# Kernel tuning notes

Hardware: AMD Instinct MI355X
Metric: run time of the kernel (lower is better)

The kernel has to match this reference:

```python
import jax, jax.numpy as jnp
import numpy as np

K = 3
STRIDE = 1
PAD = 1
DIL = 1


def setup_inputs() -> dict:
    key = jax.random.key(0)
    k1, k2, k3 = jax.random.split(key, 3)
    B, C, O, H, W = 8, 64, 64, 128, 128
    x = jax.random.normal(k1, (B, C, H, W), dtype=jnp.float32)
    # small offset-conv weights so predicted offsets stay in a sane range
    w_off = jax.random.normal(k2, (2 * K * K, C, K, K), dtype=jnp.float32) * 0.05
    b_off = jnp.zeros((2 * K * K,), dtype=jnp.float32)
    w_conv = jax.random.normal(k3, (O, C, K, K), dtype=jnp.float32) * (1.0 / np.sqrt(C * K * K))
    return {"x": x, "w_off": w_off, "b_off": b_off, "w_conv": w_conv}


def _offset_conv(x, w, b):
    y = jax.lax.conv_general_dilated(
        x, w, window_strides=(STRIDE, STRIDE),
        padding=[(PAD, PAD), (PAD, PAD)], rhs_dilation=(DIL, DIL),
        dimension_numbers=("NCHW", "OIHW", "NCHW"))
    return y + b[None, :, None, None]


def _deform_conv2d(x, offset, weight):
    # torchvision deform_conv2d v1, groups=1, offset_groups=1, no bias
    B, C, H, W = x.shape
    Ho, Wo = offset.shape[2], offset.shape[3]
    # offset channels laid out as (ky, kx, [dy, dx]) pairs
    off = offset.reshape(B, K, K, 2, Ho, Wo)
    dy, dx = off[:, :, :, 0], off[:, :, :, 1]           # [B,K,K,Ho,Wo]

    hs = (jnp.arange(Ho) * STRIDE - PAD).astype(offset.dtype)
    ws = (jnp.arange(Wo) * STRIDE - PAD).astype(offset.dtype)
    kk = (jnp.arange(K) * DIL).astype(offset.dtype)
    py = hs[None, None, None, :, None] + kk[None, :, None, None, None] + dy
    px = ws[None, None, None, None, :] + kk[None, None, :, None, None] + dx

    y0 = jnp.floor(py)
    x0 = jnp.floor(px)
    ly = py - y0
    lx = px - x0
    y0i = y0.astype(jnp.int32)
    x0i = x0.astype(jnp.int32)

    xf = x.reshape(B, C, H * W)

    def gather(yi, xi):
        valid = ((yi >= 0) & (yi < H) & (xi >= 0) & (xi < W)).astype(x.dtype)
        idx = jnp.clip(yi, 0, H - 1) * W + jnp.clip(xi, 0, W - 1)  # [B,K,K,Ho,Wo]
        idxf = idx.reshape(B, 1, -1)
        v = jnp.take_along_axis(xf, idxf, axis=2)                  # [B,C,K*K*Ho*Wo]
        v = v.reshape(B, C, K, K, Ho, Wo)
        return v * valid[:, None]                                  # zero-pad out of bounds

    ly_ = ly[:, None]  # broadcast over channel dim
    lx_ = lx[:, None]
    val = (gather(y0i, x0i) * (1 - ly_) * (1 - lx_)
           + gather(y0i, x0i + 1) * (1 - ly_) * lx_
           + gather(y0i + 1, x0i) * ly_ * (1 - lx_)
           + gather(y0i + 1, x0i + 1) * ly_ * lx_)   # [B,C,K,K,Ho,Wo]

    return jnp.einsum("bcklhw,ockl->bohw", val, weight)


def reference(x, w_off, b_off, w_conv):
    offset = _offset_conv(x, w_off, b_off)
    return _deform_conv2d(x, offset, w_conv)
```

## Files before the change

kernel.cpp:

```cpp
#include <hip/hip_runtime.h>

#define B_    8
#define C_    64
#define O_    64
#define H_    128
#define W_    128
#define HW_   (H_ * W_)
#define NOFF_ 18
#define KK_   9
#define TW_   19
#define PADW_ 5

typedef __attribute__((ext_vector_type(8))) _Float16 f16x8;
typedef __attribute__((ext_vector_type(2))) _Float16 f16x2;
typedef __attribute__((ext_vector_type(4))) unsigned int u32x4;
typedef __attribute__((ext_vector_type(4))) float f32x4;
typedef unsigned int uint32;
typedef unsigned short ushort;

__device__ __forceinline__ f16x2 u2h(uint32 u) {
    union { uint32 u; f16x2 h; } c; c.u = u; return c.h;
}
__device__ __forceinline__ f16x8 u2h8(u32x4 q) {
    union { u32x4 u; f16x8 h; } c; c.u = q; return c.h;
}

#define GLOAD16(dst, a64) \
    asm volatile("global_load_dwordx4 %0, %1, off" : "=&v"(dst) : "v"(a64) : "memory")
#define WAITV(N) do { \
    asm volatile("s_waitcnt vmcnt(" #N ")" ::: "memory"); \
    __builtin_amdgcn_sched_barrier(0); } while (0)
#define DRAIN_ALL() do { \
    asm volatile("s_waitcnt vmcnt(0) lgkmcnt(0)" ::: "memory"); \
    __builtin_amdgcn_sched_barrier(0); } while (0)

__global__ __launch_bounds__(256) void transpose_x(
    const float* __restrict__ x, _Float16* __restrict__ xT)
{
    __shared__ float tile[64][65];
    int blk = blockIdx.x;
    int b   = blk >> 8;
    int hw0 = (blk & 255) * 64;
    int t   = threadIdx.x;
    int q   = t >> 6;
    int ln  = t & 63;
#pragma unroll
    for (int p = 0; p < 16; ++p) {
        int c = p * 4 + q;
        tile[c][ln] = x[((size_t)(b * C_ + c) << 14) + hw0 + ln];
    }
    __syncthreads();
#pragma unroll
    for (int p = 0; p < 16; ++p) {
        int hw = p * 4 + q;
        xT[(((size_t)b << 14) + hw0 + hw) * 64 + ln] = (_Float16)tile[ln][hw];
    }
}

__global__ __launch_bounds__(256) void prep3(
    const float* __restrict__ w_conv, const float* __restrict__ w_off,
    _Float16* __restrict__ wfrag, _Float16* __restrict__ wofff)
{
    int idx = blockIdx.x * 256 + threadIdx.x;
    if (idx < 36864) {
        int i    = idx & 7;
        int lane = (idx >> 3) & 63;
        int nb   = (idx >> 9) & 3;
        int kc   = (idx >> 11) & 1;
        int kk   = idx >> 12;
        int c = kc * 32 + ((lane >> 4) << 3) + i;
        int o = nb * 16 + (lane & 15);
        wfrag[idx] = (_Float16)w_conv[(o * C_ + c) * 9 + kk];
    }
    if (idx < 18432) {
        int i    = idx & 7;
        int lane = (idx >> 3) & 63;
        int nb   = (idx >> 9) & 1;
        int kc   = (idx >> 10) & 1;
        int kk   = idx >> 11;
        int m = nb * 16 + (lane & 15);
        int c = kc * 32 + ((lane >> 4) << 3) + i;
        wofff[idx] = (_Float16)((m < NOFF_) ? w_off[(m * C_ + c) * 9 + kk] : 0.0f);
    }
}

__global__ __launch_bounds__(512, 2) void offconv_mfma5(
    const _Float16* __restrict__ xT, const _Float16* __restrict__ wofff,
    const float* __restrict__ b_off, _Float16* __restrict__ offsh)
{
    __shared__ _Float16 wlds[18432];
    int t = threadIdx.x;
    {
        const u32x4* src = (const u32x4*)wofff;
        u32x4* dst = (u32x4*)wlds;
#pragma unroll
        for (int r = 0; r < 5; ++r) {
            int i = r * 512 + t;
            if (i < 2304) dst[i] = src[i];
        }
    }
    DRAIN_ALL();
    __syncthreads();

    int blk  = blockIdx.x;
    int b    = blk & 7;
    int hw0  = (blk >> 3) * 128;
    int lane = t & 63;
    int wv   = t >> 6;
    int pxb  = hw0 + wv * 16;
    int pr   = lane & 15;
    int g    = lane >> 4;
    int px   = pxb + pr;
    int h = px >> 7, w = px & (W_ - 1);
    const _Float16* xb = xT + (((size_t)b << 14) << 6);

    f32x4 acc[2];
#pragma unroll
    for (int nb = 0; nb < 2; ++nb) acc[nb] = (f32x4){0.f, 0.f, 0.f, 0.f};

    u32x4 q[3][2];
    bool  vld[3];

    auto issueO = [&](int kk, int st) {
        int ky = kk / 3, kx = kk % 3;
        int yy = h - 1 + ky, xx = w - 1 + kx;
        vld[st] = ((unsigned)yy < (unsigned)H_) && ((unsigned)xx < (unsigned)W_);
        int src = (min(max(yy, 0), H_ - 1) << 7) + min(max(xx, 0), W_ - 1);
        unsigned long long a = (unsigned long long)(xb + ((size_t)src << 6) + g * 8);
        GLOAD16(q[st][0], a);
        unsigned long long a2 = a + 64;
        GLOAD16(q[st][1], a2);
    };

    issueO(0, 0); issueO(1, 1); issueO(2, 2);
#pragma unroll
    for (int kk = 0; kk < KK_; ++kk) {
        const int s = kk % 3;
        if (kk < 7)      { WAITV(4); }
        else if (kk < 8) { WAITV(2); }
        else             { WAITV(0); }
#pragma unroll
        for (int kc = 0; kc < 2; ++kc) {
            f16x8 a = u2h8(q[s][kc]);
            f16x8 z = {};
            a = vld[s] ? a : z;
#pragma unroll
            for (int nb = 0; nb < 2; ++nb) {
                f16x8 bfr = *(const f16x8*)(wlds +
                    ((((kk * 2 + kc) << 1) + nb) << 9) + (lane << 3));
                acc[nb] = __builtin_amdgcn_mfma_f32_16x16x32_f16(a, bfr, acc[nb], 0, 0, 0);
            }
        }
        if (kk < 6) issueO(kk + 3, s);
    }

#pragma unroll
    for (int nb = 0; nb < 2; ++nb) {
        int m = nb * 16 + pr;
        if (m < NOFF_) {
            float bias = b_off[m];
#pragma unroll
            for (int r = 0; r < 4; ++r) {
                int prow = pxb + g * 4 + r;
                offsh[(size_t)((b << 14) + prow) * NOFF_ + m] = (_Float16)(acc[nb][r] + bias);
            }
        }
    }
}

__global__ __launch_bounds__(256, 3) void deform_mfma9(
    const _Float16* __restrict__ xT, const _Float16* __restrict__ offsh,
    const _Float16* __restrict__ wfrag, float* __restrict__ out)
{
    __shared__ u32x4 tile4[TW_ * TW_ * 8];

    int t    = threadIdx.x;
    int blk  = blockIdx.x;
    int b    = blk & 7;
    int tid  = blk >> 3;
    int ty   = tid >> 4, tx = tid & 15;
    int lane = t & 63;
    int wv   = t >> 6;
    int pr   = lane & 15;
    int gg   = lane >> 4;
    int ry0  = ty * 8 - PADW_;
    int cx0  = tx * 8 - PADW_;
    const _Float16* xb = xT + (((size_t)b << 14) << 6);

#pragma unroll
    for (int it = 0; it < 12; ++it) {
        int idx = it * 256 + t;
        if (idx < TW_ * TW_ * 8) {
            int i   = idx / (TW_ * 8);
            int rem = idx - i * (TW_ * 8);
            int j   = rem >> 3, cg = rem & 7;
            int yy = min(max(ry0 + i, 0), H_ - 1);
            int xx = min(max(cx0 + j, 0), W_ - 1);
            u32x4 v = *(const u32x4*)(xb + (((size_t)((yy << 7) + xx)) << 6) + (cg << 3));
            int rl = i * TW_ + j;
            int bo = ((rl << 7) + (cg << 4)) ^ ((rl & 7) << 4);
            *(u32x4*)((char*)tile4 + bo) = v;
        }
    }

    int h_img = ty * 8 + wv * 2 + (pr >> 3);
    int w_img = tx * 8 + (pr & 7);
    const uint32* obu = (const uint32*)(offsh +
        (size_t)((b << 14) + (h_img << 7) + w_img) * NOFF_);
    uint32 dpk[9];
#pragma unroll
    for (int kk = 0; kk < 9; ++kk) dpk[kk] = obu[kk];
    DRAIN_ALL();
    __syncthreads();

    f32x4 acc[4];
#pragma unroll
    for (int nb = 0; nb < 4; ++nb) acc[nb] = (f32x4){0.f, 0.f, 0.f, 0.f};

    u32x4 wq[8];
    u32x4 q[8];

#pragma unroll
    for (int kk = 0; kk < KK_; ++kk) {
#pragma unroll
        for (int f = 0; f < 8; ++f) {
            unsigned long long wa = (unsigned long long)(wfrag +
                ((((kk * 2 + (f >> 2)) << 2) + (f & 3)) << 9) + (lane << 3));
            GLOAD16(wq[f], wa);
        }

        int ky = kk / 3, kx = kk % 3;
        union { uint32 u; f16x2 hh; } cv; cv.u = dpk[kk];
        float dyv = (float)cv.hh[0], dxv = (float)cv.hh[1];
        float py  = (float)(h_img - 1 + ky) + dyv;
        float pxf = (float)(w_img - 1 + kx) + dxv;
        float y0f = floorf(py), x0f = floorf(pxf);
        float ly = py - y0f, lx = pxf - x0f;
        int y0 = (int)y0f, x0 = (int)x0f;
        float w00 = (1.f - ly) * (1.f - lx);
        float w01 = (1.f - ly) * lx;
        float w10 = ly * (1.f - lx);
        float w11 = ly * lx;
        bool vy0 = (unsigned)y0       < (unsigned)H_;
        bool vy1 = (unsigned)(y0 + 1) < (unsigned)H_;
        bool vx0 = (unsigned)x0       < (unsigned)W_;
        bool vx1 = (unsigned)(x0 + 1) < (unsigned)W_;
        if (!(vy0 && vx0)) w00 = 0.f;
        if (!(vy0 && vx1)) w01 = 0.f;
        if (!(vy1 && vx0)) w10 = 0.f;
        if (!(vy1 && vx1)) w11 = 0.f;
        int yc0 = min(max(y0, 0), H_ - 1);
        int yc1 = min(max(y0 + 1, 0), H_ - 1);
        int xc0 = min(max(x0, 0), W_ - 1);
        int xc1 = min(max(x0 + 1, 0), W_ - 1);
        f16x2 Wc0 = (f16x2){(_Float16)w00, (_Float16)w00};
        f16x2 Wc1 = (f16x2){(_Float16)w01, (_Float16)w01};
        f16x2 Wc2 = (f16x2){(_Float16)w10, (_Float16)w10};
        f16x2 Wc3 = (f16x2){(_Float16)w11, (_Float16)w11};

        int r0 = yc0 - ry0, r1 = yc1 - ry0;
        int c0 = xc0 - cx0, c1 = xc1 - cx0;
        int bad = ((unsigned)r0 >= TW_) | ((unsigned)r1 >= TW_) |
                  ((unsigned)c0 >= TW_) | ((unsigned)c1 >= TW_);

        if (!__any(bad)) {
            int rl00 = r0 * TW_ + c0, rl01 = r0 * TW_ + c1;
            int rl10 = r1 * TW_ + c0, rl11 = r1 * TW_ + c1;
#pragma unroll
            for (int kc = 0; kc < 2; ++kc) {
                int ch = ((kc << 2) + gg) << 4;
                q[kc * 4 + 0] = *(const u32x4*)((char*)tile4 + (((rl00 << 7) + ch) ^ ((rl00 & 7) << 4)));
                q[kc * 4 + 1] = *(const u32x4*)((char*)tile4 + (((rl01 << 7) + ch) ^ ((rl01 & 7) << 4)));
                q[kc * 4 + 2] = *(const u32x4*)((char*)tile4 + (((rl10 << 7) + ch) ^ ((rl10 & 7) << 4)));
                q[kc * 4 + 3] = *(const u32x4*)((char*)tile4 + (((rl11 << 7) + ch) ^ ((rl11 & 7) << 4)));
            }
        } else {
#pragma unroll
            for (int kc = 0; kc < 2; ++kc) {
                int ce = ((kc << 2) + gg) << 3;
                unsigned long long a00 = (unsigned long long)(xb + (((size_t)((yc0 << 7) + xc0)) << 6) + ce);
                unsigned long long a01 = (unsigned long long)(xb + (((size_t)((yc0 << 7) + xc1)) << 6) + ce);
                unsigned long long a10 = (unsigned long long)(xb + (((size_t)((yc1 << 7) + xc0)) << 6) + ce);
                unsigned long long a11 = (unsigned long long)(xb + (((size_t)((yc1 << 7) + xc1)) << 6) + ce);
                GLOAD16(q[kc * 4 + 0], a00);
                GLOAD16(q[kc * 4 + 1], a01);
                GLOAD16(q[kc * 4 + 2], a10);
                GLOAD16(q[kc * 4 + 3], a11);
            }
        }

        WAITV(0);

#pragma unroll
        for (int kc = 0; kc < 2; ++kc) {
            f16x8 a;
            f16x2* ap = (f16x2*)&a;
#pragma unroll
            for (int p4 = 0; p4 < 4; ++p4) {
                ap[p4] = u2h(q[kc * 4 + 0][p4]) * Wc0
                       + u2h(q[kc * 4 + 1][p4]) * Wc1
                       + u2h(q[kc * 4 + 2][p4]) * Wc2
                       + u2h(q[kc * 4 + 3][p4]) * Wc3;
            }
#pragma unroll
            for (int nb = 0; nb < 4; ++nb) {
                acc[nb] = __builtin_amdgcn_mfma_f32_16x16x32_f16(
                    a, u2h8(wq[kc * 4 + nb]), acc[nb], 0, 0, 0);
            }
        }
    }

#pragma unroll
    for (int nb = 0; nb < 4; ++nb) {
        int o = nb * 16 + pr;
        int orow = ty * 8 + wv * 2 + (gg >> 1);
        int ocol = tx * 8 + ((gg & 1) << 2);
        float* outp = out + (((size_t)(b * O_ + o)) << 14) + (orow << 7) + ocol;
        *(f32x4*)outp = acc[nb];
    }
}

extern "C" void kernel_launch(void* const* d_in, const int* in_sizes, int n_in,
                              void* d_out, int out_size, void* d_ws, size_t ws_size,
                              hipStream_t stream)
{
    const float* x      = (const float*)d_in[0];
    const float* w_off  = (const float*)d_in[1];
    const float* b_off  = (const float*)d_in[2];
    const float* w_conv = (const float*)d_in[3];
    float* out = (float*)d_out;
    char* ws = (char*)d_ws;

    const size_t XT_OFF    = 0;
    const size_t OFFS_OFF  = 16777216;
    const size_t WFRAG_OFF = 21495808;
    const size_t WOFF_OFF  = 21569536;

    _Float16* xT    = (_Float16*)(ws + XT_OFF);
    _Float16* offsh = (_Float16*)(ws + OFFS_OFF);
    _Float16* wfrag = (_Float16*)(ws + WFRAG_OFF);
    _Float16* wofff = (_Float16*)(ws + WOFF_OFF);

    transpose_x  <<<2048, 256, 0, stream>>>(x, xT);
    prep3        <<<144, 256, 0, stream>>>(w_conv, w_off, wfrag, wofff);
    offconv_mfma5<<<1024, 512, 0, stream>>>(xT, wofff, b_off, offsh);
    deform_mfma9 <<<2048, 256, 0, stream>>>(xT, offsh, wfrag, out);
}
```

Measured before the change: 66.83 us.

## Widen deform tile to 8x16 pixels and split output channels across waves

The deform conv kernel now uses 512-thread blocks covering an 8x16 pixel tile. Each wave handles two pixel rows of 16 columns and half of the output channels. The weight fragments that wave needs (its 32 output channels across all 9 taps) are loaded into registers once before the loop instead of being reloaded from global memory every tap. The wider shared tile (19x26) reduces halo overhead per pixel. In exchange, register pressure rises, and the bilinear gather and interpolation are now done twice per pixel, once for each output-channel half.

```diff
diff --git a/kernel.cpp b/kernel.cpp
--- a/kernel.cpp
+++ b/kernel.cpp
@@ -8,8 +8,8 @@
 #define HW_   (H_ * W_)
 #define NOFF_ 18
 #define KK_   9
-#define TW_   19
-#define PADW_ 5
+#define TR_   19
+#define TC_   26
 
 typedef __attribute__((ext_vector_type(8))) _Float16 f16x8;
 typedef __attribute__((ext_vector_type(2))) _Float16 f16x2;
@@ -168,72 +168,74 @@
     }
 }
 
-__global__ __launch_bounds__(256, 3) void deform_mfma9(
+__global__ __launch_bounds__(512, 2) void deform_mfma11(
     const _Float16* __restrict__ xT, const _Float16* __restrict__ offsh,
     const _Float16* __restrict__ wfrag, float* __restrict__ out)
 {
-    __shared__ u32x4 tile4[TW_ * TW_ * 8];
+    __shared__ _Float16 tile_s[TR_ * TC_ * 64];
+    char* tilec = (char*)tile_s;
 
     int t    = threadIdx.x;
+    int lane = t & 63;
+    int wv   = t >> 6;
     int blk  = blockIdx.x;
     int b    = blk & 7;
     int tid  = blk >> 3;
-    int ty   = tid >> 4, tx = tid & 15;
-    int lane = t & 63;
-    int wv   = t >> 6;
-    int pr   = lane & 15;
+    int ty   = tid >> 3, tx = tid & 7;
+    int pxg  = wv & 3;
+    int oh   = wv >> 2;
+    int ry0  = ty * 8 - 5;
+    int cx0  = tx * 16 - 5;
+    int colp = lane & 15;
     int gg   = lane >> 4;
-    int ry0  = ty * 8 - PADW_;
-    int cx0  = tx * 8 - PADW_;
     const _Float16* xb = xT + (((size_t)b << 14) << 6);
 
 #pragma unroll
-    for (int it = 0; it < 12; ++it) {
-        int idx = it * 256 + t;
-        if (idx < TW_ * TW_ * 8) {
-            int i   = idx / (TW_ * 8);
-            int rem = idx - i * (TW_ * 8);
-            int j   = rem >> 3, cg = rem & 7;
-            int yy = min(max(ry0 + i, 0), H_ - 1);
-            int xx = min(max(cx0 + j, 0), W_ - 1);
+    for (int it = 0; it < 8; ++it) {
+        int idx = it * 512 + t;
+        if (idx < TR_ * TC_ * 8) {
+            int rl = idx >> 3, cg = idx & 7;
+            int r  = rl / TC_, c = rl - r * TC_;
+            int yy = min(max(ry0 + r, 0), H_ - 1);
+            int xx = min(max(cx0 + c, 0), W_ - 1);
             u32x4 v = *(const u32x4*)(xb + (((size_t)((yy << 7) + xx)) << 6) + (cg << 3));
-            int rl = i * TW_ + j;
             int bo = ((rl << 7) + (cg << 4)) ^ ((rl & 7) << 4);
-            *(u32x4*)((char*)tile4 + bo) = v;
-        }
-    }
-
-    int h_img = ty * 8 + wv * 2 + (pr >> 3);
-    int w_img = tx * 8 + (pr & 7);
-    const uint32* obu = (const uint32*)(offsh +
-        (size_t)((b << 14) + (h_img << 7) + w_img) * NOFF_);
-    uint32 dpk[9];
-#pragma unroll
-    for (int kk = 0; kk < 9; ++kk) dpk[kk] = obu[kk];
+            *(u32x4*)(tilec + bo) = v;
+        }
+    }
+
+    u32x4 wreg[9][2][2];
+#pragma unroll
+    for (int kk = 0; kk < 9; ++kk)
+#pragma unroll
+        for (int kc = 0; kc < 2; ++kc)
+#pragma unroll
+            for (int j = 0; j < 2; ++j)
+                wreg[kk][kc][j] = *(const u32x4*)(wfrag +
+                    ((((kk * 2 + kc) << 2) + oh * 2 + j) << 9) + (lane << 3));
+
+    int rowA = ty * 8 + 2 * pxg;
+    int colI = tx * 16 + colp;
+    const uint32* obuA = (const uint32*)(offsh +
+        (size_t)((b << 14) + (rowA << 7) + colI) * NOFF_);
+    const uint32* obuB = (const uint32*)(offsh +
+        (size_t)((b << 14) + ((rowA + 1) << 7) + colI) * NOFF_);
+    uint32 dpkA[9], dpkB[9];
+#pragma unroll
+    for (int kk = 0; kk < 9; ++kk) { dpkA[kk] = obuA[kk]; dpkB[kk] = obuB[kk]; }
+
     DRAIN_ALL();
     __syncthreads();
 
-    f32x4 acc[4];
-#pragma unroll
-    for (int nb = 0; nb < 4; ++nb) acc[nb] = (f32x4){0.f, 0.f, 0.f, 0.f};
-
-    u32x4 wq[8];
-    u32x4 q[8];
-
-#pragma unroll
-    for (int kk = 0; kk < KK_; ++kk) {
-#pragma unroll
-        for (int f = 0; f < 8; ++f) {
-            unsigned long long wa = (unsigned long long)(wfrag +
-                ((((kk * 2 + (f >> 2)) << 2) + (f & 3)) << 9) + (lane << 3));
-            GLOAD16(wq[f], wa);
-        }
-
-        int ky = kk / 3, kx = kk % 3;
-        union { uint32 u; f16x2 hh; } cv; cv.u = dpk[kk];
+    f32x4 acc00 = {0.f,0.f,0.f,0.f}, acc01 = {0.f,0.f,0.f,0.f};
+    f32x4 acc10 = {0.f,0.f,0.f,0.f}, acc11 = {0.f,0.f,0.f,0.f};
+
+    auto prepPx = [&](uint32 du, int row_img, int col_img, int ky, int kx,
+                      f16x2* Wc, int* rl, int* yc, int* xc) -> int {
+        union { uint32 u; f16x2 hh; } cv; cv.u = du;
         float dyv = (float)cv.hh[0], dxv = (float)cv.hh[1];
-        float py  = (float)(h_img - 1 + ky) + dyv;
-        float pxf = (float)(w_img - 1 + kx) + dxv;
+        float py  = (float)(row_img - 1 + ky) + dyv;
+        float pxf = (float)(col_img - 1 + kx) + dxv;
         float y0f = floorf(py), x0f = floorf(pxf);
         float ly = py - y0f, lx = pxf - x0f;
         int y0 = (int)y0f, x0 = (int)x0f;
@@ -253,70 +255,86 @@
         int yc1 = min(max(y0 + 1, 0), H_ - 1);
         int xc0 = min(max(x0, 0), W_ - 1);
         int xc1 = min(max(x0 + 1, 0), W_ - 1);
-        f16x2 Wc0 = (f16x2){(_Float16)w00, (_Float16)w00};
-        f16x2 Wc1 = (f16x2){(_Float16)w01, (_Float16)w01};
-        f16x2 Wc2 = (f16x2){(_Float16)w10, (_Float16)w10};
-        f16x2 Wc3 = (f16x2){(_Float16)w11, (_Float16)w11};
-
+        Wc[0] = (f16x2){(_Float16)w00, (_Float16)w00};
+        Wc[1] = (f16x2){(_Float16)w01, (_Float16)w01};
+        Wc[2] = (f16x2){(_Float16)w10, (_Float16)w10};
+        Wc[3] = (f16x2){(_Float16)w11, (_Float16)w11};
+        yc[0] = yc0; yc[1] = yc1; xc[0] = xc0; xc[1] = xc1;
         int r0 = yc0 - ry0, r1 = yc1 - ry0;
         int c0 = xc0 - cx0, c1 = xc1 - cx0;
-        int bad = ((unsigned)r0 >= TW_) | ((unsigned)r1 >= TW_) |
-                  ((unsigned)c0 >= TW_) | ((unsigned)c1 >= TW_);
-
-        if (!__any(bad)) {
-            int rl00 = r0 * TW_ + c0, rl01 = r0 * TW_ + c1;
-            int rl10 = r1 * TW_ + c0, rl11 = r1 * TW_ + c1;
+        rl[0] = r0 * TC_ + c0; rl[1] = r0 * TC_ + c1;
+        rl[2] = r1 * TC_ + c0; rl[3] = r1 * TC_ + c1;
+        return ((unsigned)r0 >= TR_ - 1) | ((unsigned)r1 >= TR_) |
+               ((unsigned)c0 >= TC_ - 1) | ((unsigned)c1 >= TC_);
+    };
+
+#pragma unroll
+    for (int kk = 0; kk < KK_; ++kk) {
+        const int ky = kk / 3, kx = kk % 3;
+
+#pragma unroll
+        for (int mt = 0; mt < 2; ++mt) {
+            f16x2 Wc[4]; int rl[4], yc[2], xc[2];
+            int bad = prepPx(mt ? dpkB[kk] : dpkA[kk], rowA + mt, colI, ky, kx,
+                             Wc, rl, yc, xc);
+            u32x4 q[8];
+            if (!__any(bad)) {
+#pragma unroll
+                for (int kc = 0; kc < 2; ++kc) {
+                    int ch = ((kc << 2) + gg) << 4;
+#pragma unroll
+                    for (int cr = 0; cr < 4; ++cr) {
+                        int bo = (((rl[cr]) << 7) + ch) ^ ((rl[cr] & 7) << 4);
+                        q[kc * 4 + cr] = *(const u32x4*)(tilec + bo);
+                    }
+                }
+            } else {
+#pragma unroll
+                for (int kc = 0; kc < 2; ++kc) {
+                    int ce = ((kc << 2) + gg) << 3;
+#pragma unroll
+                    for (int cr = 0; cr < 4; ++cr) {
+                        int yy = yc[cr >> 1], xx = xc[cr & 1];
+                        unsigned long long a = (unsigned long long)(xb +
+                            (((size_t)((yy << 7) + xx)) << 6) + ce);
+                        GLOAD16(q[kc * 4 + cr], a);
+                    }
+                }
+                WAITV(0);
+            }
 #pragma unroll
             for (int kc = 0; kc < 2; ++kc) {
-                int ch = ((kc << 2) + gg) << 4;
-                q[kc * 4 + 0] = *(const u32x4*)((char*)tile4 + (((rl00 << 7) + ch) ^ ((rl00 & 7) << 4)));
-                q[kc * 4 + 1] = *(const u32x4*)((char*)tile4 + (((rl01 << 7) + ch) ^ ((rl01 & 7) << 4)));
-                q[kc * 4 + 2] = *(const u32x4*)((char*)tile4 + (((rl10 << 7) + ch) ^ ((rl10 & 7) << 4)));
-                q[kc * 4 + 3] = *(const u32x4*)((char*)tile4 + (((rl11 << 7) + ch) ^ ((rl11 & 7) << 4)));
+                f16x8 a;
+                f16x2* ap = (f16x2*)&a;
+#pragma unroll
+                for (int p4 = 0; p4 < 4; ++p4) {
+                    ap[p4] = u2h(q[kc * 4 + 0][p4]) * Wc[0]
+                           + u2h(q[kc * 4 + 1][p4]) * Wc[1]
+                           + u2h(q[kc * 4 + 2][p4]) * Wc[2]
+                           + u2h(q[kc * 4 + 3][p4]) * Wc[3];
+                }
+                if (mt == 0) {
+                    acc00 = __builtin_amdgcn_mfma_f32_16x16x32_f16(a, u2h8(wreg[kk][kc][0]), acc00, 0, 0, 0);
+                    acc01 = __builtin_amdgcn_mfma_f32_16x16x32_f16(a, u2h8(wreg[kk][kc][1]), acc01, 0, 0, 0);
+                } else {
+                    acc10 = __builtin_amdgcn_mfma_f32_16x16x32_f16(a, u2h8(wreg[kk][kc][0]), acc10, 0, 0, 0);
+                    acc11 = __builtin_amdgcn_mfma_f32_16x16x32_f16(a, u2h8(wreg[kk][kc][1]), acc11, 0, 0, 0);
+                }
             }
-        } else {
-#pragma unroll
-            for (int kc = 0; kc < 2; ++kc) {
-                int ce = ((kc << 2) + gg) << 3;
-                unsigned long long a00 = (unsigned long long)(xb + (((size_t)((yc0 << 7) + xc0)) << 6) + ce);
-                unsigned long long a01 = (unsigned long long)(xb + (((size_t)((yc0 << 7) + xc1)) << 6) + ce);
-                unsigned long long a10 = (unsigned long long)(xb + (((size_t)((yc1 << 7) + xc0)) << 6) + ce);
-                unsigned long long a11 = (unsigned long long)(xb + (((size_t)((yc1 << 7) + xc1)) << 6) + ce);
-                GLOAD16(q[kc * 4 + 0], a00);
-                GLOAD16(q[kc * 4 + 1], a01);
-                GLOAD16(q[kc * 4 + 2], a10);
-                GLOAD16(q[kc * 4 + 3], a11);
-            }
-        }
-
-        WAITV(0);
-
-#pragma unroll
-        for (int kc = 0; kc < 2; ++kc) {
-            f16x8 a;
-            f16x2* ap = (f16x2*)&a;
-#pragma unroll
-            for (int p4 = 0; p4 < 4; ++p4) {
-                ap[p4] = u2h(q[kc * 4 + 0][p4]) * Wc0
-                       + u2h(q[kc * 4 + 1][p4]) * Wc1
-                       + u2h(q[kc * 4 + 2][p4]) * Wc2
-                       + u2h(q[kc * 4 + 3][p4]) * Wc3;
-            }
-#pragma unroll
-            for (int nb = 0; nb < 4; ++nb) {
-                acc[nb] = __builtin_amdgcn_mfma_f32_16x16x32_f16(
-                    a, u2h8(wq[kc * 4 + nb]), acc[nb], 0, 0, 0);
-            }
-        }
-    }
-
-#pragma unroll
-    for (int nb = 0; nb < 4; ++nb) {
-        int o = nb * 16 + pr;
-        int orow = ty * 8 + wv * 2 + (gg >> 1);
-        int ocol = tx * 8 + ((gg & 1) << 2);
-        float* outp = out + (((size_t)(b * O_ + o)) << 14) + (orow << 7) + ocol;
-        *(f32x4*)outp = acc[nb];
+        }
+    }
+
+    int ocol0 = tx * 16 + (gg << 2);
+#pragma unroll
+    for (int mt = 0; mt < 2; ++mt) {
+        int orow = rowA + mt;
+#pragma unroll
+        for (int j = 0; j < 2; ++j) {
+            int o = oh * 32 + j * 16 + colp;
+            f32x4 v = mt ? (j ? acc11 : acc10) : (j ? acc01 : acc00);
+            float* outp = out + (((size_t)(b * O_ + o)) << 14) + (orow << 7) + ocol0;
+            *(f32x4*)outp = v;
+        }
     }
 }
 
@@ -344,5 +362,5 @@
     transpose_x  <<<2048, 256, 0, stream>>>(x, xT);
     prep3        <<<144, 256, 0, stream>>>(w_conv, w_off, wfrag, wofff);
     offconv_mfma5<<<1024, 512, 0, stream>>>(xT, wofff, b_off, offsh);
-    deform_mfma9 <<<2048, 256, 0, stream>>>(xT, offsh, wfrag, out);
-}
+    deform_mfma11<<<1024, 512, 0, stream>>>(xT, offsh, wfrag, out);
+}
```

After: 86.61 us. 1.3x slower.

## Double-buffer weight fragment loads and use padded LDS row stride in deform kernel

Applied to the files above, without the earlier changes.

Prefetches the next kernel-tap's weight fragments into a second register buffer while the current tap's bilinear gather and MFMAs run, waiting with a partial vmcnt instead of draining all loads. Also replaces the XOR-swizzled LDS tile layout with a padded 144-byte row stride to avoid bank conflicts with simpler addressing. This costs extra VGPRs for the second weight buffer and more LDS per block, which may pressure occupancy at three blocks per CU.

```diff
diff --git a/kernel.cpp b/kernel.cpp
--- a/kernel.cpp
+++ b/kernel.cpp
@@ -10,6 +10,7 @@
 #define KK_   9
 #define TW_   19
 #define PADW_ 5
+#define RSTR_ 144
 
 typedef __attribute__((ext_vector_type(8))) _Float16 f16x8;
 typedef __attribute__((ext_vector_type(2))) _Float16 f16x2;
@@ -27,6 +28,10 @@
 
 #define GLOAD16(dst, a64) \
     asm volatile("global_load_dwordx4 %0, %1, off" : "=&v"(dst) : "v"(a64) : "memory")
+#define WAITV_TIE(N, w) \
+    asm volatile("s_waitcnt vmcnt(" #N ")" \
+        : "+v"(w[0]), "+v"(w[1]), "+v"(w[2]), "+v"(w[3]), \
+          "+v"(w[4]), "+v"(w[5]), "+v"(w[6]), "+v"(w[7]))
 #define WAITV(N) do { \
     asm volatile("s_waitcnt vmcnt(" #N ")" ::: "memory"); \
     __builtin_amdgcn_sched_barrier(0); } while (0)
@@ -168,11 +173,11 @@
     }
 }
 
-__global__ __launch_bounds__(256, 3) void deform_mfma9(
+__global__ __launch_bounds__(256, 3) void deform_mfma10(
     const _Float16* __restrict__ xT, const _Float16* __restrict__ offsh,
     const _Float16* __restrict__ wfrag, float* __restrict__ out)
 {
-    __shared__ u32x4 tile4[TW_ * TW_ * 8];
+    __shared__ char tilec[TW_ * TW_ * RSTR_];
 
     int t    = threadIdx.x;
     int blk  = blockIdx.x;
@@ -198,8 +203,7 @@
             int xx = min(max(cx0 + j, 0), W_ - 1);
             u32x4 v = *(const u32x4*)(xb + (((size_t)((yy << 7) + xx)) << 6) + (cg << 3));
             int rl = i * TW_ + j;
-            int bo = ((rl << 7) + (cg << 4)) ^ ((rl & 7) << 4);
-            *(u32x4*)((char*)tile4 + bo) = v;
+            *(u32x4*)(tilec + rl * RSTR_ + (cg << 4)) = v;
         }
     }
 
@@ -217,17 +221,24 @@
 #pragma unroll
     for (int nb = 0; nb < 4; ++nb) acc[nb] = (f32x4){0.f, 0.f, 0.f, 0.f};
 
-    u32x4 wq[8];
+    u32x4 wqA[8], wqB[8];
     u32x4 q[8];
 
-#pragma unroll
-    for (int kk = 0; kk < KK_; ++kk) {
+    auto issueW = [&](int kk, u32x4* wq) {
 #pragma unroll
         for (int f = 0; f < 8; ++f) {
             unsigned long long wa = (unsigned long long)(wfrag +
                 ((((kk * 2 + (f >> 2)) << 2) + (f & 3)) << 9) + (lane << 3));
             GLOAD16(wq[f], wa);
         }
+    };
+
+    issueW(0, wqA);
+#pragma unroll
+    for (int kk = 0; kk < KK_; ++kk) {
+        u32x4* wcur = (kk & 1) ? wqB : wqA;
+        u32x4* wnxt = (kk & 1) ? wqA : wqB;
+        if (kk < 8) issueW(kk + 1, wnxt);
 
         int ky = kk / 3, kx = kk % 3;
         union { uint32 u; f16x2 hh; } cv; cv.u = dpk[kk];
@@ -266,13 +277,14 @@
         if (!__any(bad)) {
             int rl00 = r0 * TW_ + c0, rl01 = r0 * TW_ + c1;
             int rl10 = r1 * TW_ + c0, rl11 = r1 * TW_ + c1;
+            int ch0 = gg << 4;
 #pragma unroll
             for (int kc = 0; kc < 2; ++kc) {
-                int ch = ((kc << 2) + gg) << 4;
-                q[kc * 4 + 0] = *(const u32x4*)((char*)tile4 + (((rl00 << 7) + ch) ^ ((rl00 & 7) << 4)));
-                q[kc * 4 + 1] = *(const u32x4*)((char*)tile4 + (((rl01 << 7) + ch) ^ ((rl01 & 7) << 4)));
-                q[kc * 4 + 2] = *(const u32x4*)((char*)tile4 + (((rl10 << 7) + ch) ^ ((rl10 & 7) << 4)));
-                q[kc * 4 + 3] = *(const u32x4*)((char*)tile4 + (((rl11 << 7) + ch) ^ ((rl11 & 7) << 4)));
+                int ch = ch0 + (kc << 6);
+                q[kc * 4 + 0] = *(const u32x4*)(tilec + rl00 * RSTR_ + ch);
+                q[kc * 4 + 1] = *(const u32x4*)(tilec + rl01 * RSTR_ + ch);
+                q[kc * 4 + 2] = *(const u32x4*)(tilec + rl10 * RSTR_ + ch);
+                q[kc * 4 + 3] = *(const u32x4*)(tilec + rl11 * RSTR_ + ch);
             }
         } else {
 #pragma unroll
@@ -287,9 +299,10 @@
                 GLOAD16(q[kc * 4 + 2], a10);
                 GLOAD16(q[kc * 4 + 3], a11);
             }
-        }
-
-        WAITV(0);
+            WAITV(0);
+        }
+
+        if (kk < 8) { WAITV_TIE(8, wcur); } else { WAITV_TIE(0, wcur); }
 
 #pragma unroll
         for (int kc = 0; kc < 2; ++kc) {
@@ -305,7 +318,7 @@
 #pragma unroll
             for (int nb = 0; nb < 4; ++nb) {
                 acc[nb] = __builtin_amdgcn_mfma_f32_16x16x32_f16(
-                    a, u2h8(wq[kc * 4 + nb]), acc[nb], 0, 0, 0);
+                    a, u2h8(wcur[kc * 4 + nb]), acc[nb], 0, 0, 0);
             }
         }
     }
@@ -344,5 +357,5 @@
     transpose_x  <<<2048, 256, 0, stream>>>(x, xT);
     prep3        <<<144, 256, 0, stream>>>(w_conv, w_off, wfrag, wofff);
     offconv_mfma5<<<1024, 512, 0, stream>>>(xT, wofff, b_off, offsh);
-    deform_mfma9 <<<2048, 256, 0, stream>>>(xT, offsh, wfrag, out);
-}
+    deform_mfma10<<<2048, 256, 0, stream>>>(xT, offsh, wfrag, out);
+}
```

Result: no change. 65.63 us, median of 2 (-1.8%).
